# Kernel tuning notes

Measured on AMD Instinct MI355X. Metric: run time of the kernel, lower is better.

## Reference

```python
import jax, jax.numpy as jnp
import numpy as np

N = 50000   # num_of_nodes (cfg.dataset.num_nodes)
C = 128     # in_channels; TopKPooling ratio = C/N -> k = C pooled nodes
E = 800000  # num edges


def setup_inputs() -> dict:
    key = jax.random.key(0)
    ks = jax.random.split(key, 8)
    std = 1.0 / np.sqrt(C)
    X = jax.random.normal(ks[0], (N, C), dtype=jnp.float32)
    edge_index = jax.random.randint(ks[1], (2, E), 0, N, dtype=jnp.int64)
    edge_weight = jax.random.uniform(ks[2], (E,), dtype=jnp.float32)
    p = jax.random.normal(ks[3], (C,), dtype=jnp.float32)                      # TopKPooling projection
    W_ih = jax.random.normal(ks[4], (3 * C, C), dtype=jnp.float32) * std       # GRU input weights [r|z|n]
    W_hh = jax.random.normal(ks[5], (3 * C, C), dtype=jnp.float32) * std       # GRU hidden weights
    b_ih = jnp.zeros((3 * C,), dtype=jnp.float32)
    b_hh = jnp.zeros((3 * C,), dtype=jnp.float32)
    W_conv = jax.random.uniform(ks[6], (C, C), dtype=jnp.float32, minval=-std, maxval=std)  # GCN lin weight
    b_conv = jnp.zeros((C,), dtype=jnp.float32)
    return {"X": X, "edge_weight": edge_weight, "p": p, "W_ih": W_ih, "W_hh": W_hh,
            "b_ih": b_ih, "b_hh": b_hh, "W_conv": W_conv, "b_conv": b_conv,
            "edge_index": edge_index}


def _forward(X, edge_weight, p, W_ih, W_hh, b_ih, b_hh, W_conv, b_conv, edge_index):
    # ---- TopKPooling: score = X.p/||p||, pick top k=C nodes, gate with tanh ----
    score = X @ p / jnp.linalg.norm(p)                       # [N]
    top_vals, top_idx = jax.lax.top_k(score, C)              # k = C (ratio = C/N)
    X_tilde = X[top_idx] * jnp.tanh(top_vals)[:, None]       # [C, C]
    X_tilde = jax.lax.stop_gradient(X_tilde)                 # .detach() in original

    # ---- GRU single step: input X_tilde (batch=C), hidden h0 = W_conv ----
    gi = X_tilde @ W_ih.T + b_ih                             # [C, 3C]
    gh = W_conv @ W_hh.T + b_hh                              # [C, 3C]
    gi_r, gi_z, gi_n = jnp.split(gi, 3, axis=-1)
    gh_r, gh_z, gh_n = jnp.split(gh, 3, axis=-1)
    r = jax.nn.sigmoid(gi_r + gh_r)
    z = jax.nn.sigmoid(gi_z + gh_z)
    n = jnp.tanh(gi_n + r * gh_n)
    W_new = (1.0 - z) * n + z * W_conv                       # evolved GCN weight [C, C]

    # ---- GCNConv with self-loops + symmetric normalization ----
    src, dst = edge_index[0], edge_index[1]
    loop = jnp.arange(N, dtype=src.dtype)
    src2 = jnp.concatenate([src, loop])
    dst2 = jnp.concatenate([dst, loop])
    w2 = jnp.concatenate([edge_weight, jnp.ones((N,), dtype=edge_weight.dtype)])
    deg = jax.ops.segment_sum(w2, dst2, num_segments=N)      # [N]
    dinv = jnp.where(deg > 0, jax.lax.rsqrt(deg), 0.0)
    norm = dinv[src2] * w2 * dinv[dst2]                      # [E+N]
    Xw = X @ W_new.T                                         # [N, C]
    msg = Xw[src2] * norm[:, None]                           # gather + scale, [E+N, C]
    out = jax.ops.segment_sum(msg, dst2, num_segments=N)     # scatter-add, [N, C]
    return out + b_conv


def reference(X, edge_weight, p, W_ih, W_hh, b_ih, b_hh, W_conv, b_conv, edge_index):
    return _forward(X, edge_weight, p, W_ih, W_hh, b_ih, b_hh, W_conv, b_conv, edge_index)
```

## Files before the change

kernel.cpp:

```cpp
#include <hip/hip_runtime.h>
#include <hip/hip_fp16.h>
#include <math.h>

#define C 128
#define HB 2048
#define NS 4096
#define SHB 128

typedef __attribute__((ext_vector_type(8))) short bf16x8;
typedef __attribute__((ext_vector_type(4))) float f32x4;

__device__ inline unsigned ord_f32(float f) {
    unsigned u = __float_as_uint(f);
    return u ^ ((u & 0x80000000u) ? 0xFFFFFFFFu : 0x80000000u);
}
__device__ inline float unord_f32(unsigned u) {
    return __uint_as_float(u ^ ((u & 0x80000000u) ? 0x80000000u : 0xFFFFFFFFu));
}
__device__ inline short f2bf(float f) {
    unsigned u = __float_as_uint(f);
    return (short)((u + 0x7FFFu + ((u >> 16) & 1u)) >> 16);
}
__device__ inline float bf2f(short s) {
    return __uint_as_float(((unsigned)(unsigned short)s) << 16);
}

__global__ __launch_bounds__(1024) void k_front(const float* __restrict__ X,
                                                const float* __restrict__ p,
                                                float* __restrict__ scores,
                                                int* __restrict__ hist,
                                                const int* __restrict__ ei,
                                                int* __restrict__ rh,
                                                int N, int E, int NBIN, int NBLKE) {
    int t = threadIdx.x;
    if (blockIdx.x < SHB) {
        __shared__ int lh[HB];
        for (int i = t; i < HB; i += 1024) lh[i] = 0;
        __syncthreads();
        int gw   = blockIdx.x * 16 + (t >> 6);
        int lane = t & 63;
        for (int r = gw; r < N; r += 2048) {
            const float* xr = X + (size_t)r * C;
            float a = xr[lane] * p[lane] + xr[lane + 64] * p[lane + 64];
            #pragma unroll
            for (int o = 32; o; o >>= 1) a += __shfl_down(a, o);
            if (lane == 0) {
                scores[r] = a;
                atomicAdd(&lh[ord_f32(a) >> 21], 1);
            }
        }
        __syncthreads();
        for (int i = t; i < HB; i += 1024) {
            int v = lh[i];
            if (v) atomicAdd(&hist[i], v);
        }
    } else {
        __shared__ int bh[256];
        for (int i = t; i < 256; i += 1024) bh[i] = 0;
        __syncthreads();
        int eb = blockIdx.x - SHB;
        int e = eb * 2048 + t * 2;
        if (e + 1 < E) {
            int2 d2 = *(const int2*)(ei + E + e);
            atomicAdd(&bh[d2.x >> 8], 1);
            atomicAdd(&bh[d2.y >> 8], 1);
        } else if (e < E) {
            atomicAdd(&bh[ei[E + e] >> 8], 1);
        }
        __syncthreads();
        for (int i = t; i < NBIN; i += 1024) rh[(size_t)i * NBLKE + eb] = bh[i];
    }
}

__global__ __launch_bounds__(512) void k_rscanA(int* __restrict__ rh, int* __restrict__ tot, int NBLKE) {
    __shared__ int sc[512];
    int t = threadIdx.x;
    int bin = blockIdx.x;
    int v = (t < NBLKE) ? rh[(size_t)bin * NBLKE + t] : 0;
    sc[t] = v;
    __syncthreads();
    for (int off = 1; off < 512; off <<= 1) {
        int u = (t >= off) ? sc[t - off] : 0;
        __syncthreads();
        sc[t] += u;
        __syncthreads();
    }
    if (t < NBLKE) rh[(size_t)bin * NBLKE + t] = sc[t] - v;
    if (t == 511) tot[bin] = sc[511];
}

__global__ __launch_bounds__(256) void k_rscanB(const int* __restrict__ tot, int* __restrict__ binbase,
                                                int NBIN, int E) {
    __shared__ int sc[256];
    int t = threadIdx.x;
    int v = (t < NBIN) ? tot[t] : 0;
    sc[t] = v;
    __syncthreads();
    for (int off = 1; off < 256; off <<= 1) {
        int u = (t >= off) ? sc[t - off] : 0;
        __syncthreads();
        sc[t] += u;
        __syncthreads();
    }
    if (t < NBIN) binbase[t] = sc[t] - v;
    if (t == 0) binbase[NBIN] = E;
}

__global__ __launch_bounds__(1024) void k_rscat(const int* __restrict__ ei, const float* __restrict__ ew,
                                                const int* __restrict__ rh, const int* __restrict__ binbase,
                                                unsigned long long* __restrict__ sorted,
                                                int E, int NBIN, int NBLKE) {
    __shared__ int cur[256];
    int t = threadIdx.x;
    int eb = blockIdx.x;
    for (int i = t; i < NBIN; i += 1024) cur[i] = binbase[i] + rh[(size_t)i * NBLKE + eb];
    __syncthreads();
    int e = eb * 2048 + t * 2;
    #pragma unroll
    for (int j = 0; j < 2; j++) {
        int ee = e + j;
        if (ee < E) {
            int s = ei[ee], d = ei[E + ee];
            float w = ew[ee];
            int pos = atomicAdd(&cur[d >> 8], 1);
            unsigned long long pk = ((unsigned long long)(unsigned)d << 48)
                                  | ((unsigned long long)(unsigned short)s << 32)
                                  |  (unsigned long long)__float_as_uint(w);
            sorted[pos] = pk;
        }
    }
}

__global__ __launch_bounds__(1024) void k_bin(const unsigned long long* __restrict__ sorted,
                                              const int* __restrict__ binbase,
                                              int* __restrict__ offs, float* __restrict__ dinv,
                                              unsigned* __restrict__ epack,
                                              int N, int E, int NBIN) {
    __shared__ int cnt[256];
    __shared__ float wsum[256];
    __shared__ int sc[256];
    __shared__ int cur2[256];
    int t = threadIdx.x;
    int b = blockIdx.x;
    int s0 = binbase[b], s1 = binbase[b + 1];
    for (int i = t; i < 256; i += 1024) { cnt[i] = 0; wsum[i] = 0.f; }
    __syncthreads();
    for (int i = s0 + t; i < s1; i += 1024) {
        unsigned long long pk = sorted[i];
        int d8 = (int)(pk >> 48) & 255;
        float w = __uint_as_float((unsigned)(pk & 0xFFFFFFFFull));
        atomicAdd(&cnt[d8], 1);
        atomicAdd(&wsum[d8], w);
    }
    __syncthreads();
    int v = (t < 256) ? cnt[t] : 0;
    if (t < 256) sc[t] = v;
    __syncthreads();
    for (int off = 1; off < 256; off <<= 1) {
        int u = (t < 256 && t >= off) ? sc[t - off] : 0;
        __syncthreads();
        if (t < 256) sc[t] += u;
        __syncthreads();
    }
    if (t < 256) {
        int loff = sc[t] - v;
        cur2[t] = s0 + loff;
        int node = b * 256 + t;
        if (node < N) {
            offs[node] = s0 + loff;
            dinv[node] = rsqrtf(1.0f + wsum[t]);
        }
    }
    if (b == NBIN - 1 && t == 0) offs[N] = E;
    __syncthreads();
    for (int i = s0 + t; i < s1; i += 1024) {
        unsigned long long pk = sorted[i];
        int d8 = (int)(pk >> 48) & 255;
        unsigned src = (unsigned)((pk >> 32) & 0xFFFFu);
        float w = __uint_as_float((unsigned)(pk & 0xFFFFFFFFull));
        int pos = atomicAdd(&cur2[d8], 1);
        __half hw = __float2half(w);
        epack[pos] = ((unsigned)*(unsigned short*)&hw << 16) | src;
    }
}

__global__ __launch_bounds__(256) void k_filter(const float* __restrict__ scores,
                                                const int* __restrict__ hist,
                                                int* __restrict__ nc,
                                                unsigned long long* __restrict__ cand, int N) {
    __shared__ int sc[256];
    __shared__ int sT;
    int t = threadIdx.x;
    int loc[8];
    int sum = 0;
    #pragma unroll
    for (int s = 0; s < 8; s++) {
        loc[s] = hist[HB - 1 - (t * 8 + s)];
        sum += loc[s];
    }
    sc[t] = sum;
    __syncthreads();
    for (int off = 1; off < 256; off <<= 1) {
        int v = (t >= off) ? sc[t - off] : 0;
        __syncthreads();
        sc[t] += v;
        __syncthreads();
    }
    int run = sc[t] - sum;
    #pragma unroll
    for (int s = 0; s < 8; s++) {
        int b = HB - 1 - (t * 8 + s);
        int nr = run + loc[s];
        if (run < C && nr >= C) sT = b;
        run = nr;
    }
    __syncthreads();
    int T = sT;
    int i = blockIdx.x * 256 + t;
    if (i < N) {
        unsigned u = ord_f32(scores[i]);
        if ((int)(u >> 21) >= T) {
            int pos = atomicAdd(nc, 1);
            if (pos < NS)
                cand[pos] = ((unsigned long long)u << 32) | (unsigned)(~(unsigned)i);
        }
    }
}

__global__ __launch_bounds__(1024) void k_sel(const unsigned long long* __restrict__ cand,
                                              const int* __restrict__ nc,
                                              const float* __restrict__ p,
                                              int* __restrict__ tidx, float* __restrict__ gate) {
    __shared__ unsigned long long sk[NS];
    __shared__ float red[16];
    __shared__ float s_pn;
    int t = threadIdx.x;
    int M = *nc; if (M > NS) M = NS;
    int S = 256; while (S < M) S <<= 1;
    for (int i = t; i < S; i += 1024) sk[i] = (i < M) ? cand[i] : 0ULL;
    float pv = 0.f;
    if (t < C) { float x = p[t]; pv = x * x; }
    #pragma unroll
    for (int o = 32; o; o >>= 1) pv += __shfl_down(pv, o);
    if ((t & 63) == 0) red[t >> 6] = pv;
    __syncthreads();
    if (t == 0) {
        float s = 0.f;
        for (int i = 0; i < 16; i++) s += red[i];
        s_pn = sqrtf(s);
    }
    for (int k = 2; k <= S; k <<= 1) {
        for (int j = k >> 1; j > 0; j >>= 1) {
            __syncthreads();
            for (int idx = t; idx < S; idx += 1024) {
                int l = idx ^ j;
                if (l > idx) {
                    unsigned long long a = sk[idx], b = sk[l];
                    bool desc = (idx & k) == 0;
                    if (desc ? (a < b) : (a > b)) { sk[idx] = b; sk[l] = a; }
                }
            }
        }
    }
    __syncthreads();
    if (t < C) {
        unsigned long long g = sk[t];
        tidx[t] = (int)(~(unsigned)(g & 0xFFFFFFFFull));
        gate[t] = tanhf(unord_f32((unsigned)(g >> 32)) / s_pn);
    }
}

__global__ __launch_bounds__(256) void k_gru(const float* __restrict__ X,
                                             const int* __restrict__ tidx,
                                             const float* __restrict__ gate,
                                             const float* __restrict__ Wc,
                                             const float* __restrict__ W_ih, const float* __restrict__ W_hh,
                                             const float* __restrict__ b_ih, const float* __restrict__ b_hh,
                                             float* __restrict__ wnewT) {
    int t = threadIdx.x;
    int i = t & 127;
    int j = blockIdx.x * 2 + (t >> 7);
    int src = tidx[i];
    float g = gate[i];
    const float4* xr   = (const float4*)(X + (size_t)src * C);
    const float4* hr   = (const float4*)(Wc + (size_t)i * C);
    const float4* wri  = (const float4*)(W_ih + (size_t)j * C);
    const float4* wzi  = (const float4*)(W_ih + (size_t)(C + j) * C);
    const float4* wni  = (const float4*)(W_ih + (size_t)(2 * C + j) * C);
    const float4* wrh  = (const float4*)(W_hh + (size_t)j * C);
    const float4* wzh  = (const float4*)(W_hh + (size_t)(C + j) * C);
    const float4* wnh  = (const float4*)(W_hh + (size_t)(2 * C + j) * C);
    float gir = 0, giz = 0, gin = 0, ghr = 0, ghz = 0, ghn = 0;
    #pragma unroll 8
    for (int k4 = 0; k4 < C / 4; k4++) {
        float4 x = xr[k4], h = hr[k4], a;
        a = wri[k4]; gir += x.x * a.x + x.y * a.y + x.z * a.z + x.w * a.w;
        a = wzi[k4]; giz += x.x * a.x + x.y * a.y + x.z * a.z + x.w * a.w;
        a = wni[k4]; gin += x.x * a.x + x.y * a.y + x.z * a.z + x.w * a.w;
        a = wrh[k4]; ghr += h.x * a.x + h.y * a.y + h.z * a.z + h.w * a.w;
        a = wzh[k4]; ghz += h.x * a.x + h.y * a.y + h.z * a.z + h.w * a.w;
        a = wnh[k4]; ghn += h.x * a.x + h.y * a.y + h.z * a.z + h.w * a.w;
    }
    gir = g * gir + b_ih[j];         ghr += b_hh[j];
    giz = g * giz + b_ih[C + j];     ghz += b_hh[C + j];
    gin = g * gin + b_ih[2 * C + j]; ghn += b_hh[2 * C + j];
    float r = 1.f / (1.f + expf(-(gir + ghr)));
    float z = 1.f / (1.f + expf(-(giz + ghz)));
    float n = tanhf(gin + r * ghn);
    float wn = (1.f - z) * n + z * Wc[(size_t)i * C + j];
    wnewT[(size_t)j * C + i] = wn;
}

__global__ __launch_bounds__(256) void k_xw(const float* __restrict__ X,
                                            const float* __restrict__ wnewT,
                                            const float* __restrict__ dinv,
                                            unsigned* __restrict__ xwh, int N) {
    __shared__ short Bh[C * C];
    __shared__ short Bl[C * C];
    int t = threadIdx.x;
    for (int idx = t; idx < C * C; idx += 256) {
        int k = idx >> 7, c = idx & 127;
        float wv = wnewT[idx];
        short hi = f2bf(wv);
        float lo = wv - bf2f(hi);
        int pos = c * C + (k ^ ((c & 15) << 3));
        Bh[pos] = hi;
        Bl[pos] = f2bf(lo);
    }
    __syncthreads();

    int wave = t >> 6, lane = t & 63;
    int ln = lane & 15, quad = lane >> 4;
    int r0 = blockIdx.x * 128 + wave * 32;

    f32x4 acc[2][8];
    #pragma unroll
    for (int mt = 0; mt < 2; mt++)
        #pragma unroll
        for (int ct = 0; ct < 8; ct++) { acc[mt][ct][0] = 0.f; acc[mt][ct][1] = 0.f; acc[mt][ct][2] = 0.f; acc[mt][ct][3] = 0.f; }

    int row0 = r0 + ln;       if (row0 >= N) row0 = N - 1;
    int row1 = r0 + 16 + ln;  if (row1 >= N) row1 = N - 1;
    const float* xr0 = X + (size_t)row0 * C + quad * 8;
    const float* xr1 = X + (size_t)row1 * C + quad * 8;

    for (int ks = 0; ks < 4; ks++) {
        float a0[8], a1[8];
        *(float4*)&a0[0] = *(const float4*)(xr0 + ks * 32);
        *(float4*)&a0[4] = *(const float4*)(xr0 + ks * 32 + 4);
        *(float4*)&a1[0] = *(const float4*)(xr1 + ks * 32);
        *(float4*)&a1[4] = *(const float4*)(xr1 + ks * 32 + 4);
        bf16x8 a0h, a0l, a1h, a1l;
        #pragma unroll
        for (int j = 0; j < 8; j++) {
            short h0 = f2bf(a0[j]); a0h[j] = h0; a0l[j] = f2bf(a0[j] - bf2f(h0));
            short h1 = f2bf(a1[j]); a1h[j] = h1; a1l[j] = f2bf(a1[j] - bf2f(h1));
        }
        int kb = ks * 32 + quad * 8;
        int koff = kb ^ (ln << 3);
        #pragma unroll
        for (int ct = 0; ct < 8; ct++) {
            int pos = (ct * 16 + ln) * C + koff;
            bf16x8 bh = *(bf16x8*)&Bh[pos];
            bf16x8 bl = *(bf16x8*)&Bl[pos];
            acc[0][ct] = __builtin_amdgcn_mfma_f32_16x16x32_bf16(a0h, bh, acc[0][ct], 0, 0, 0);
            acc[0][ct] = __builtin_amdgcn_mfma_f32_16x16x32_bf16(a0l, bh, acc[0][ct], 0, 0, 0);
            acc[0][ct] = __builtin_amdgcn_mfma_f32_16x16x32_bf16(a0h, bl, acc[0][ct], 0, 0, 0);
            acc[1][ct] = __builtin_amdgcn_mfma_f32_16x16x32_bf16(a1h, bh, acc[1][ct], 0, 0, 0);
            acc[1][ct] = __builtin_amdgcn_mfma_f32_16x16x32_bf16(a1l, bh, acc[1][ct], 0, 0, 0);
            acc[1][ct] = __builtin_amdgcn_mfma_f32_16x16x32_bf16(a1h, bl, acc[1][ct], 0, 0, 0);
        }
    }

    __half* H = (__half*)xwh;
    #pragma unroll
    for (int mt = 0; mt < 2; mt++) {
        int rbase = r0 + mt * 16 + quad * 4;
        #pragma unroll
        for (int reg = 0; reg < 4; reg++) {
            int r = rbase + reg;
            if (r < N) {
                float dvr = dinv[r];
                #pragma unroll
                for (int ct = 0; ct < 8; ct++) {
                    int col = ct * 16 + ln;
                    H[(size_t)r * C + col] = __float2half(acc[mt][ct][reg] * dvr);
                }
            }
        }
    }
}

__global__ __launch_bounds__(256) void k_gather(const unsigned* __restrict__ xwh,
                                                const int* __restrict__ offs,
                                                const unsigned* __restrict__ epack,
                                                const float* __restrict__ dinv,
                                                const float* __restrict__ b_conv,
                                                float* __restrict__ out, int N) {
    int t = threadIdx.x;
    int v = blockIdx.x * 4 + (t >> 6);
    int lane = t & 63;
    if (v >= N) return;
    float dv = dinv[v];
    unsigned uv = xwh[(size_t)v * 64 + lane];
    __half2 hv = *(__half2*)&uv;
    float acc0 = __low2float(hv);
    float acc1 = __high2float(hv);
    int e0 = offs[v], e1 = offs[v + 1];
    int e = e0;
    for (; e + 7 < e1; e += 8) {
        unsigned pk[8], ux[8];
        #pragma unroll
        for (int j = 0; j < 8; j++) pk[j] = __builtin_nontemporal_load(&epack[e + j]);
        #pragma unroll
        for (int j = 0; j < 8; j++) ux[j] = xwh[(size_t)(pk[j] & 0xFFFFu) * 64 + lane];
        #pragma unroll
        for (int j = 0; j < 8; j++) {
            unsigned short hs = (unsigned short)(pk[j] >> 16);
            float nm = __half2float(*(__half*)&hs);
            __half2 h = *(__half2*)&ux[j];
            acc0 += nm * __low2float(h);
            acc1 += nm * __high2float(h);
        }
    }
    for (; e + 3 < e1; e += 4) {
        unsigned pk[4], ux[4];
        #pragma unroll
        for (int j = 0; j < 4; j++) pk[j] = __builtin_nontemporal_load(&epack[e + j]);
        #pragma unroll
        for (int j = 0; j < 4; j++) ux[j] = xwh[(size_t)(pk[j] & 0xFFFFu) * 64 + lane];
        #pragma unroll
        for (int j = 0; j < 4; j++) {
            unsigned short hs = (unsigned short)(pk[j] >> 16);
            float nm = __half2float(*(__half*)&hs);
            __half2 h = *(__half2*)&ux[j];
            acc0 += nm * __low2float(h);
            acc1 += nm * __high2float(h);
        }
    }
    for (; e < e1; e++) {
        unsigned pA = __builtin_nontemporal_load(&epack[e]);
        unsigned uA = xwh[(size_t)(pA & 0xFFFFu) * 64 + lane];
        unsigned short hs = (unsigned short)(pA >> 16);
        float nA = __half2float(*(__half*)&hs);
        __half2 hA = *(__half2*)&uA;
        acc0 += nA * __low2float(hA);
        acc1 += nA * __high2float(hA);
    }
    const float2* b2 = (const float2*)b_conv;
    float2 bb = b2[lane];
    unsigned long long ov = ((unsigned long long)__float_as_uint(acc1 * dv + bb.y) << 32)
                          |  (unsigned long long)__float_as_uint(acc0 * dv + bb.x);
    __builtin_nontemporal_store(ov, (unsigned long long*)(out + (size_t)v * C) + lane);
}

extern "C" void kernel_launch(void* const* d_in, const int* in_sizes, int n_in,
                              void* d_out, int out_size, void* d_ws, size_t ws_size,
                              hipStream_t stream) {
    const float* X      = (const float*)d_in[0];
    const float* ew     = (const float*)d_in[1];
    const float* p      = (const float*)d_in[2];
    const float* W_ih   = (const float*)d_in[3];
    const float* W_hh   = (const float*)d_in[4];
    const float* b_ih   = (const float*)d_in[5];
    const float* b_hh   = (const float*)d_in[6];
    const float* W_conv = (const float*)d_in[7];
    const float* b_conv = (const float*)d_in[8];
    const int*   ei     = (const int*)d_in[9];
    const int N = in_sizes[0] / C;
    const int E = in_sizes[1];
    float* out = (float*)d_out;
    const int NB    = (N + 255) / 256;
    const int NBIN  = (N + 255) / 256;
    const int NBLKE = (E + 2047) / 2048;

    char* w = (char*)d_ws;
    auto alloc = [&](size_t bytes) -> void* {
        void* r = (void*)w;
        w += (bytes + 255) & ~(size_t)255;
        return r;
    };
    int*   hist   = (int*)alloc(HB * 4);
    int*   nc     = (int*)alloc(256);
    size_t zbytes = (size_t)(w - (char*)d_ws);
    float* scores = (float*)alloc((size_t)N * 4);
    float* dinv   = (float*)alloc((size_t)N * 4);
    int*   offs   = (int*)alloc((size_t)(N + 1) * 4);
    int*   rh     = (int*)alloc((size_t)NBIN * NBLKE * 4);
    int*   tot    = (int*)alloc((size_t)NBIN * 4);
    int*   binbase= (int*)alloc((size_t)(NBIN + 1) * 4);
    unsigned long long* cand = (unsigned long long*)alloc((size_t)NS * 8);
    int*   tidx   = (int*)alloc(C * 4);
    float* gate   = (float*)alloc(C * 4);
    float* wnewT  = (float*)alloc((size_t)C * C * 4);
    unsigned long long* sorted = (unsigned long long*)alloc((size_t)E * 8);
    unsigned* epack = (unsigned*)alloc((size_t)E * 4);
    unsigned* xwh = (unsigned*)alloc((size_t)N * 64 * 4);

    hipMemsetAsync(d_ws, 0, zbytes, stream);
    k_front<<<SHB + NBLKE, 1024, 0, stream>>>(X, p, scores, hist, ei, rh, N, E, NBIN, NBLKE);
    k_filter<<<NB, 256, 0, stream>>>(scores, hist, nc, cand, N);
    k_sel<<<1, 1024, 0, stream>>>(cand, nc, p, tidx, gate);
    k_gru<<<C / 2, 256, 0, stream>>>(X, tidx, gate, W_conv, W_ih, W_hh, b_ih, b_hh, wnewT);
    k_rscanA<<<NBIN, 512, 0, stream>>>(rh, tot, NBLKE);
    k_rscanB<<<1, 256, 0, stream>>>(tot, binbase, NBIN, E);
    k_rscat<<<NBLKE, 1024, 0, stream>>>(ei, ew, rh, binbase, sorted, E, NBIN, NBLKE);
    k_bin<<<NBIN, 1024, 0, stream>>>(sorted, binbase, offs, dinv, epack, N, E, NBIN);
    k_xw<<<(N + 127) / 128, 256, 0, stream>>>(X, wnewT, dinv, xwh, N);
    k_gather<<<(N + 3) / 4, 256, 0, stream>>>(xwh, offs, epack, dinv, b_conv, out, N);
}
```

Baseline: 226.4 us.

## Fold bin-base scan into scatter and bin kernels, privatize edge histogram

Removes the single-block k_rscanB launch. Each k_rscat and k_bin block now recomputes the 256-entry exclusive scan of bin totals in shared memory. The edge-bin histogram in k_front is split into 8 shared-memory copies to reduce atomic contention, and the score pass uses more blocks with float2 loads. This saves one kernel launch and its serialization gap, at the cost of redundant per-block scans.

```diff
diff --git a/kernel.cpp b/kernel.cpp
--- a/kernel.cpp
+++ b/kernel.cpp
@@ -5,7 +5,7 @@
 #define C 128
 #define HB 2048
 #define NS 4096
-#define SHB 128
+#define SHB 192
 
 typedef __attribute__((ext_vector_type(8))) short bf16x8;
 typedef __attribute__((ext_vector_type(4))) float f32x4;
@@ -39,9 +39,12 @@
         __syncthreads();
         int gw   = blockIdx.x * 16 + (t >> 6);
         int lane = t & 63;
-        for (int r = gw; r < N; r += 2048) {
-            const float* xr = X + (size_t)r * C;
-            float a = xr[lane] * p[lane] + xr[lane + 64] * p[lane + 64];
+        const float2* p2 = (const float2*)p;
+        float2 pv2 = p2[lane];
+        for (int r = gw; r < N; r += SHB * 16) {
+            const float2* xr = (const float2*)(X + (size_t)r * C);
+            float2 x2 = xr[lane];
+            float a = x2.x * pv2.x + x2.y * pv2.y;
             #pragma unroll
             for (int o = 32; o; o >>= 1) a += __shfl_down(a, o);
             if (lane == 0) {
@@ -55,20 +58,26 @@
             if (v) atomicAdd(&hist[i], v);
         }
     } else {
-        __shared__ int bh[256];
-        for (int i = t; i < 256; i += 1024) bh[i] = 0;
+        __shared__ int bh[8][256];
+        int cp = (t >> 7) & 7;
+        for (int i = t; i < 8 * 256; i += 1024) ((int*)bh)[i] = 0;
         __syncthreads();
         int eb = blockIdx.x - SHB;
         int e = eb * 2048 + t * 2;
         if (e + 1 < E) {
             int2 d2 = *(const int2*)(ei + E + e);
-            atomicAdd(&bh[d2.x >> 8], 1);
-            atomicAdd(&bh[d2.y >> 8], 1);
+            atomicAdd(&bh[cp][d2.x >> 8], 1);
+            atomicAdd(&bh[cp][d2.y >> 8], 1);
         } else if (e < E) {
-            atomicAdd(&bh[ei[E + e] >> 8], 1);
-        }
-        __syncthreads();
-        for (int i = t; i < NBIN; i += 1024) rh[(size_t)i * NBLKE + eb] = bh[i];
+            atomicAdd(&bh[cp][ei[E + e] >> 8], 1);
+        }
+        __syncthreads();
+        for (int i = t; i < NBIN; i += 1024) {
+            int s = 0;
+            #pragma unroll
+            for (int c = 0; c < 8; c++) s += bh[c][i];
+            rh[(size_t)i * NBLKE + eb] = s;
+        }
     }
 }
 
@@ -89,31 +98,27 @@
     if (t == 511) tot[bin] = sc[511];
 }
 
-__global__ __launch_bounds__(256) void k_rscanB(const int* __restrict__ tot, int* __restrict__ binbase,
-                                                int NBIN, int E) {
-    __shared__ int sc[256];
-    int t = threadIdx.x;
-    int v = (t < NBIN) ? tot[t] : 0;
-    sc[t] = v;
-    __syncthreads();
-    for (int off = 1; off < 256; off <<= 1) {
-        int u = (t >= off) ? sc[t - off] : 0;
-        __syncthreads();
-        sc[t] += u;
-        __syncthreads();
-    }
-    if (t < NBIN) binbase[t] = sc[t] - v;
-    if (t == 0) binbase[NBIN] = E;
-}
-
 __global__ __launch_bounds__(1024) void k_rscat(const int* __restrict__ ei, const float* __restrict__ ew,
-                                                const int* __restrict__ rh, const int* __restrict__ binbase,
+                                                const int* __restrict__ rh, const int* __restrict__ tot,
                                                 unsigned long long* __restrict__ sorted,
                                                 int E, int NBIN, int NBLKE) {
+    __shared__ int sc[256];
     __shared__ int cur[256];
     int t = threadIdx.x;
     int eb = blockIdx.x;
-    for (int i = t; i < NBIN; i += 1024) cur[i] = binbase[i] + rh[(size_t)i * NBLKE + eb];
+    int v = 0;
+    if (t < 256) {
+        v = (t < NBIN) ? tot[t] : 0;
+        sc[t] = v;
+    }
+    __syncthreads();
+    for (int off = 1; off < 256; off <<= 1) {
+        int u = (t < 256 && t >= off) ? sc[t - off] : 0;
+        __syncthreads();
+        if (t < 256) sc[t] += u;
+        __syncthreads();
+    }
+    if (t < NBIN) cur[t] = (sc[t] - v) + rh[(size_t)t * NBLKE + eb];
     __syncthreads();
     int e = eb * 2048 + t * 2;
     #pragma unroll
@@ -132,7 +137,7 @@
 }
 
 __global__ __launch_bounds__(1024) void k_bin(const unsigned long long* __restrict__ sorted,
-                                              const int* __restrict__ binbase,
+                                              const int* __restrict__ tot,
                                               int* __restrict__ offs, float* __restrict__ dinv,
                                               unsigned* __restrict__ epack,
                                               int N, int E, int NBIN) {
@@ -140,9 +145,24 @@
     __shared__ float wsum[256];
     __shared__ int sc[256];
     __shared__ int cur2[256];
+    __shared__ int s_base[2];
     int t = threadIdx.x;
     int b = blockIdx.x;
-    int s0 = binbase[b], s1 = binbase[b + 1];
+    int v = 0;
+    if (t < 256) {
+        v = (t < NBIN) ? tot[t] : 0;
+        sc[t] = v;
+    }
+    __syncthreads();
+    for (int off = 1; off < 256; off <<= 1) {
+        int u = (t < 256 && t >= off) ? sc[t - off] : 0;
+        __syncthreads();
+        if (t < 256) sc[t] += u;
+        __syncthreads();
+    }
+    if (t == b) { s_base[0] = sc[t] - v; s_base[1] = sc[t]; }
+    __syncthreads();
+    int s0 = s_base[0], s1 = s_base[1];
     for (int i = t; i < 256; i += 1024) { cnt[i] = 0; wsum[i] = 0.f; }
     __syncthreads();
     for (int i = s0 + t; i < s1; i += 1024) {
@@ -153,8 +173,8 @@
         atomicAdd(&wsum[d8], w);
     }
     __syncthreads();
-    int v = (t < 256) ? cnt[t] : 0;
-    if (t < 256) sc[t] = v;
+    int cv = (t < 256) ? cnt[t] : 0;
+    if (t < 256) sc[t] = cv;
     __syncthreads();
     for (int off = 1; off < 256; off <<= 1) {
         int u = (t < 256 && t >= off) ? sc[t - off] : 0;
@@ -163,7 +183,7 @@
         __syncthreads();
     }
     if (t < 256) {
-        int loff = sc[t] - v;
+        int loff = sc[t] - cv;
         cur2[t] = s0 + loff;
         int node = b * 256 + t;
         if (node < N) {
@@ -488,7 +508,6 @@
     int*   offs   = (int*)alloc((size_t)(N + 1) * 4);
     int*   rh     = (int*)alloc((size_t)NBIN * NBLKE * 4);
     int*   tot    = (int*)alloc((size_t)NBIN * 4);
-    int*   binbase= (int*)alloc((size_t)(NBIN + 1) * 4);
     unsigned long long* cand = (unsigned long long*)alloc((size_t)NS * 8);
     int*   tidx   = (int*)alloc(C * 4);
     float* gate   = (float*)alloc(C * 4);
@@ -503,9 +522,8 @@
     k_sel<<<1, 1024, 0, stream>>>(cand, nc, p, tidx, gate);
     k_gru<<<C / 2, 256, 0, stream>>>(X, tidx, gate, W_conv, W_ih, W_hh, b_ih, b_hh, wnewT);
     k_rscanA<<<NBIN, 512, 0, stream>>>(rh, tot, NBLKE);
-    k_rscanB<<<1, 256, 0, stream>>>(tot, binbase, NBIN, E);
-    k_rscat<<<NBLKE, 1024, 0, stream>>>(ei, ew, rh, binbase, sorted, E, NBIN, NBLKE);
-    k_bin<<<NBIN, 1024, 0, stream>>>(sorted, binbase, offs, dinv, epack, N, E, NBIN);
+    k_rscat<<<NBLKE, 1024, 0, stream>>>(ei, ew, rh, tot, sorted, E, NBIN, NBLKE);
+    k_bin<<<NBIN, 1024, 0, stream>>>(sorted, tot, offs, dinv, epack, N, E, NBIN);
     k_xw<<<(N + 127) / 128, 256, 0, stream>>>(X, wnewT, dinv, xwh, N);
     k_gather<<<(N + 3) / 4, 256, 0, stream>>>(xwh, offs, epack, dinv, b_conv, out, N);
 }
```

Result: no change. 224.5 us (-0.8%).
